# Optimization experiments

Measured on AMD Instinct MI355X. Metric: run time of the kernel, lower is better.

## Reference

```python
import jax, jax.numpy as jnp
import numpy as np

N_NODES = 50000
N_EDGES = 800000
IN_CH = 64
HID = 64
EDGE_DIM = 16


def _glorot(key, shape):
    fan_in, fan_out = shape[0], shape[1]
    lim = (6.0 / (fan_in + fan_out)) ** 0.5
    return jax.random.uniform(key, shape, jnp.float32, -lim, lim)


def setup_inputs() -> dict:
    key = jax.random.key(0)
    ks = jax.random.split(key, 12)
    x = jax.random.normal(ks[0], (N_NODES, IN_CH), jnp.float32)
    edge_index = jax.random.randint(ks[1], (2, N_EDGES), 0, N_NODES, jnp.int64)
    edge_attr = jax.random.normal(ks[2], (N_EDGES, EDGE_DIM), jnp.float32)
    # SAGEConv1: lin_l (aggregated neighbors, with bias) + lin_r (root, no bias)
    W1l = _glorot(ks[3], (IN_CH, HID)); b1l = jnp.zeros((HID,), jnp.float32)
    W1r = _glorot(ks[4], (IN_CH, HID))
    # SAGEConv2
    W2l = _glorot(ks[5], (HID, HID)); b2l = jnp.zeros((HID,), jnp.float32)
    W2r = _glorot(ks[6], (HID, HID))
    # edge MLP: Linear(2*HID+EDGE_DIM -> HID), ReLU, Linear(HID -> 1)
    Wm1 = _glorot(ks[7], (2 * HID + EDGE_DIM, HID))
    bm1 = jnp.zeros((HID,), jnp.float32)
    Wm2 = _glorot(ks[8], (HID, 1))
    bm2 = jnp.zeros((1,), jnp.float32)
    return dict(x=x, edge_index=edge_index, edge_attr=edge_attr,
                W1l=W1l, b1l=b1l, W1r=W1r,
                W2l=W2l, b2l=b2l, W2r=W2r,
                Wm1=Wm1, bm1=bm1, Wm2=Wm2, bm2=bm2)


def _sage_conv(x, src, dst, deg_inv, Wl, bl, Wr):
    # mean aggregation of source-node features at destination nodes
    n = x.shape[0]
    agg = jax.ops.segment_sum(x[src], dst, num_segments=n)  # [N, d]
    agg = agg * deg_inv  # mean over incoming edges
    return agg @ Wl + bl + x @ Wr


def reference(x, edge_index, edge_attr, W1l, b1l, W1r, W2l, b2l, W2r, Wm1, bm1, Wm2, bm2):
    src, dst = edge_index[0], edge_index[1]
    n = x.shape[0]
    # in-degree (over dst), clamped to 1 as in PyG mean aggregation
    deg = jax.ops.segment_sum(jnp.ones((src.shape[0],), x.dtype), dst, num_segments=n)
    deg_inv = (1.0 / jnp.maximum(deg, 1.0))[:, None]  # [N,1]

    h = jax.nn.relu(_sage_conv(x, src, dst, deg_inv, W1l, b1l, W1r))
    h = jax.nn.relu(_sage_conv(h, src, dst, deg_inv, W2l, b2l, W2r))

    # gather endpoint embeddings + concat with edge features -> MLP score
    edge_input = jnp.concatenate([h[src], h[dst], edge_attr], axis=-1)  # [E, 2H+De]
    hidden = jax.nn.relu(edge_input @ Wm1 + bm1)
    return (hidden @ Wm2 + bm2).squeeze(-1)  # [E]
```

## Files before the change

### kernel.cpp

```cpp
#include <hip/hip_runtime.h>
#include <hip/hip_bf16.h>


#define C 64
#define KP 168
#define SK 136
#define TILE_E 64

typedef short short8 __attribute__((ext_vector_type(8)));
typedef float f32x4 __attribute__((ext_vector_type(4)));

__device__ __forceinline__ unsigned short f2bf(float f) {
    unsigned int u = __float_as_uint(f);
    return (unsigned short)((u + 0x7FFFu + ((u >> 16) & 1u)) >> 16);
}
__device__ __forceinline__ unsigned int pack2(float lo, float hi) {
    return (unsigned int)f2bf(lo) | ((unsigned int)f2bf(hi) << 16);
}
__device__ __forceinline__ float bflo(unsigned int u) { return __uint_as_float(u << 16); }
__device__ __forceinline__ float bfhi(unsigned int u) { return __uint_as_float(u & 0xFFFF0000u); }

__global__ void prep(const int* __restrict__ dst, int* __restrict__ degi,
                     const float* __restrict__ ea, unsigned short* __restrict__ eaB,
                     const float* __restrict__ x, unsigned short* __restrict__ xB,
                     int E, int nx8, int doEa) {
    int i = blockIdx.x * blockDim.x + threadIdx.x;
    if (i < E) atomicAdd(&degi[dst[i]], 1);
    if (doEa && i < 2 * E) {
        const float4* p = (const float4*)(ea + (size_t)i * 8);
        float4 a = p[0], b = p[1];
        uint4 o;
        o.x = pack2(a.x, a.y); o.y = pack2(a.z, a.w);
        o.z = pack2(b.x, b.y); o.w = pack2(b.z, b.w);
        *(uint4*)(eaB + (size_t)i * 8) = o;
    }
    if (i < nx8) {
        const float4* p = (const float4*)(x + (size_t)i * 8);
        float4 a = p[0], b = p[1];
        uint4 o;
        o.x = pack2(a.x, a.y); o.y = pack2(a.z, a.w);
        o.z = pack2(b.x, b.y); o.w = pack2(b.z, b.w);
        *(uint4*)(xB + (size_t)i * 8) = o;
    }
}

__global__ __launch_bounds__(256) void scan_partial(const int* __restrict__ degi,
        int* __restrict__ rowptr, int* __restrict__ partials, int N) {
    __shared__ int sWs[4];
    int t = threadIdx.x, b = blockIdx.x;
    int g0 = b * 1024 + t * 4;
    int v0 = (g0 + 0 < N) ? degi[g0 + 0] : 0;
    int v1 = (g0 + 1 < N) ? degi[g0 + 1] : 0;
    int v2 = (g0 + 2 < N) ? degi[g0 + 2] : 0;
    int v3 = (g0 + 3 < N) ? degi[g0 + 3] : 0;
    int tsum = v0 + v1 + v2 + v3;
    int lane = t & 63, w = t >> 6;
    int incl = tsum;
    #pragma unroll
    for (int m = 1; m < 64; m <<= 1) {
        int y = __shfl_up(incl, m, 64);
        if (lane >= m) incl += y;
    }
    if (lane == 63) sWs[w] = incl;
    __syncthreads();
    int wprefix = 0;
    for (int i = 0; i < w; ++i) wprefix += sWs[i];
    int run = wprefix + incl - tsum;
    if (g0 + 0 < N) rowptr[g0 + 0] = run; run += v0;
    if (g0 + 1 < N) rowptr[g0 + 1] = run; run += v1;
    if (g0 + 2 < N) rowptr[g0 + 2] = run; run += v2;
    if (g0 + 3 < N) rowptr[g0 + 3] = run;
    if (t == 255) partials[b] = wprefix + incl;
}

__global__ __launch_bounds__(256) void scan_add_fused(int* __restrict__ rowptr,
        const int* __restrict__ partials, int* __restrict__ cursor,
        const int* __restrict__ degi, float* __restrict__ deg_inv,
        int N, int E, int nb) {
    __shared__ int sOff[64];
    int t = threadIdx.x;
    if (t < 64) {
        int v = (t < nb) ? partials[t] : 0;
        int incl = v;
        #pragma unroll
        for (int m = 1; m < 64; m <<= 1) {
            int y = __shfl_up(incl, m, 64);
            if (t >= m) incl += y;
        }
        sOff[t] = incl - v;
    }
    __syncthreads();
    int i = blockIdx.x * 256 + t;
    if (i < N) {
        int r = rowptr[i] + sOff[i >> 10];
        rowptr[i] = r;
        cursor[i] = r;
        deg_inv[i] = 1.0f / fmaxf((float)degi[i], 1.0f);
    }
    if (i == 0) rowptr[N] = E;
}

__global__ void fill_csr(const int* __restrict__ src, const int* __restrict__ dst,
                         int* __restrict__ cursor, int* __restrict__ eSrc, int E) {
    int e = blockIdx.x * blockDim.x + threadIdx.x;
    if (e < E) {
        int p = atomicAdd(&cursor[dst[e]], 1);
        eSrc[p] = src[e];
    }
}

__global__ __launch_bounds__(256) void fused_layer(
        const unsigned short* __restrict__ fB,
        const int* __restrict__ rowptr, const int* __restrict__ eSrc,
        const float* __restrict__ deg_inv,
        const float* __restrict__ Wl, const float* __restrict__ Wr,
        const float* __restrict__ bl, unsigned short* __restrict__ hOut, int N) {
    __shared__ unsigned short sW[C * SK];
    __shared__ unsigned short sAB[C * SK];
    int t = threadIdx.x;
    int lane = t & 63, w = t >> 6;
    int l15 = lane & 15, quad = lane >> 4;
    int n0 = blockIdx.x * 64;

    for (int i = t; i < 128 * C; i += 256) {
        int k = i >> 6, n = i & 63;
        float v = (k < C) ? Wl[k * C + n] : Wr[(k - C) * C + n];
        sW[n * SK + k] = f2bf(v);
    }
    for (int i = t; i < 64 * 8; i += 256) {
        int r = i >> 3, ch = i & 7;
        int node = n0 + r;
        uint4 v = {0u, 0u, 0u, 0u};
        if (node < N) v = *(const uint4*)(fB + (size_t)node * C + ch * 8);
        *(uint4*)&sAB[r * SK + 64 + ch * 8] = v;
    }

    int s8 = lane >> 3, ci = lane & 7;
    for (int p = 0; p < 16; ++p) {
        int node = n0 + w * 16 + p;
        if (node >= N) break;
        int row = rowptr[node], end = rowptr[node + 1];
        float a[8] = {0.f, 0.f, 0.f, 0.f, 0.f, 0.f, 0.f, 0.f};
        int j = row;
        for (; j + 16 <= end; j += 16) {
            int sA = eSrc[j + s8];
            int sB = eSrc[j + 8 + s8];
            uint4 vA = *(const uint4*)(fB + (size_t)sA * C + ci * 8);
            uint4 vB = *(const uint4*)(fB + (size_t)sB * C + ci * 8);
            a[0] += bflo(vA.x); a[1] += bfhi(vA.x);
            a[2] += bflo(vA.y); a[3] += bfhi(vA.y);
            a[4] += bflo(vA.z); a[5] += bfhi(vA.z);
            a[6] += bflo(vA.w); a[7] += bfhi(vA.w);
            a[0] += bflo(vB.x); a[1] += bfhi(vB.x);
            a[2] += bflo(vB.y); a[3] += bfhi(vB.y);
            a[4] += bflo(vB.z); a[5] += bfhi(vB.z);
            a[6] += bflo(vB.w); a[7] += bfhi(vB.w);
        }
        for (; j < end; j += 8) {
            if (j + s8 < end) {
                int s = eSrc[j + s8];
                uint4 v = *(const uint4*)(fB + (size_t)s * C + ci * 8);
                a[0] += bflo(v.x); a[1] += bfhi(v.x);
                a[2] += bflo(v.y); a[3] += bfhi(v.y);
                a[4] += bflo(v.z); a[5] += bfhi(v.z);
                a[6] += bflo(v.w); a[7] += bfhi(v.w);
            }
        }
        #pragma unroll
        for (int m = 8; m < 64; m <<= 1)
            #pragma unroll
            for (int k = 0; k < 8; ++k)
                a[k] += __shfl_xor(a[k], m, 64);
        if (s8 == 0) {
            float di = deg_inv[node];
            uint4 o;
            o.x = pack2(a[0] * di, a[1] * di);
            o.y = pack2(a[2] * di, a[3] * di);
            o.z = pack2(a[4] * di, a[5] * di);
            o.w = pack2(a[6] * di, a[7] * di);
            *(uint4*)&sAB[(w * 16 + p) * SK + ci * 8] = o;
        }
    }
    __syncthreads();

    short8 bW[4][4];
    #pragma unroll
    for (int t4 = 0; t4 < 4; ++t4)
        #pragma unroll
        for (int kc = 0; kc < 4; ++kc)
            bW[t4][kc] = *(const short8*)&sW[(t4 * 16 + l15) * SK + kc * 32 + quad * 8];
    float blr[4];
    #pragma unroll
    for (int t4 = 0; t4 < 4; ++t4) blr[t4] = bl[t4 * 16 + l15];

    f32x4 acc[4] = {{0.f, 0.f, 0.f, 0.f}, {0.f, 0.f, 0.f, 0.f},
                    {0.f, 0.f, 0.f, 0.f}, {0.f, 0.f, 0.f, 0.f}};
    #pragma unroll
    for (int kc = 0; kc < 4; ++kc) {
        short8 a = *(const short8*)&sAB[(w * 16 + l15) * SK + kc * 32 + quad * 8];
        #pragma unroll
        for (int t4 = 0; t4 < 4; ++t4)
            acc[t4] = __builtin_amdgcn_mfma_f32_16x16x32_bf16(a, bW[t4][kc], acc[t4], 0, 0, 0);
    }
    __syncthreads();

    #pragma unroll
    for (int t4 = 0; t4 < 4; ++t4)
        #pragma unroll
        for (int r = 0; r < 4; ++r) {
            int rl = w * 16 + quad * 4 + r;
            sW[rl * 72 + t4 * 16 + l15] = f2bf(fmaxf(acc[t4][r] + blr[t4], 0.f));
        }
    __syncthreads();
    for (int i = t; i < 64 * 8; i += 256) {
        int r = i >> 3, c8 = i & 7;
        int node = n0 + r;
        if (node < N)
            *(uint4*)(hOut + (size_t)node * C + c8 * 8) = *(const uint4*)&sW[r * 72 + c8 * 8];
    }
}

template <bool EAB>
__device__ __forceinline__ void gather_rows(const unsigned short* __restrict__ hB,
        const unsigned short* __restrict__ eaB, const float* __restrict__ ea,
        int s, int d, int idxc, int quad,
        uint4& u0, uint4& u1, uint4& u2, uint4& u3, uint4& u4) {
    const uint4* ps = (const uint4*)(hB + (size_t)s * C);
    const uint4* pd = (const uint4*)(hB + (size_t)d * C);
    u0 = ps[quad];
    u1 = ps[4 + quad];
    u2 = pd[quad];
    u3 = pd[4 + quad];
    u4.x = 0u; u4.y = 0u; u4.z = 0u; u4.w = 0u;
    if (quad < 2) {
        if (EAB) {
            u4 = *(const uint4*)(eaB + (size_t)idxc * 16 + quad * 8);
        } else {
            const float4* pe = (const float4*)(ea + (size_t)idxc * 16 + quad * 8);
            float4 f0 = pe[0], f1 = pe[1];
            u4.x = pack2(f0.x, f0.y); u4.y = pack2(f0.z, f0.w);
            u4.z = pack2(f1.x, f1.y); u4.w = pack2(f1.z, f1.w);
        }
    }
}

template <bool EAB>
__global__ __launch_bounds__(256) void edge_mlp_pipe(
        const unsigned short* __restrict__ hB, const int* __restrict__ src,
        const int* __restrict__ dst, const float* __restrict__ ea,
        const unsigned short* __restrict__ eaB,
        const float* __restrict__ Wm1, const float* __restrict__ bm1,
        const float* __restrict__ Wm2, const float* __restrict__ bm2,
        float* __restrict__ out, int E, int nTiles) {
    __shared__ unsigned short sW[C * KP];
    int t = threadIdx.x;
    int lane = t & 63, w = t >> 6;
    int l15 = lane & 15, quad = lane >> 4;

    for (int i = t; i < C * 3; i += 256) {
        int r = i / 3, cc = 144 + (i % 3) * 8;
        uint4 z = {0u, 0u, 0u, 0u};
        *(uint4*)&sW[r * KP + cc] = z;
    }
    for (int i = t; i < 144 * C; i += 256) {
        int k = i >> 6, n = i & 63;
        sW[n * KP + k] = f2bf(Wm1[i]);
    }
    __syncthreads();

    short8 bW[4][5];
    #pragma unroll
    for (int t4 = 0; t4 < 4; ++t4)
        #pragma unroll
        for (int kc = 0; kc < 5; ++kc)
            bW[t4][kc] = *(const short8*)&sW[(t4 * 16 + l15) * KP + kc * 32 + quad * 8];
    float bmr[4], w2r[4];
    #pragma unroll
    for (int t4 = 0; t4 < 4; ++t4) {
        int j = t4 * 16 + l15;
        bmr[t4] = bm1[j];
        w2r[t4] = Wm2[j];
    }
    float bb = bm2[0];

    int stride = gridDim.x;
    int lbase = w * 16 + l15;

    int tile = blockIdx.x;
    int idxc = min(tile * TILE_E + lbase, E - 1);
    int s = src[idxc], d = dst[idxc];
    int tileN = tile + stride;
    int idxNc = (tileN < nTiles) ? min(tileN * TILE_E + lbase, E - 1) : idxc;
    int sN = src[idxNc], dN = dst[idxNc];
    uint4 cu0, cu1, cu2, cu3, cu4;
    gather_rows<EAB>(hB, eaB, ea, s, d, idxc, quad, cu0, cu1, cu2, cu3, cu4);

    while (true) {
        bool hasNext = (tileN < nTiles);
        uint4 nu0, nu1, nu2, nu3, nu4;
        gather_rows<EAB>(hB, eaB, ea, sN, dN, idxNc, quad, nu0, nu1, nu2, nu3, nu4);
        int tileNN = tileN + stride;
        int idxNNc = (tileNN < nTiles) ? min(tileNN * TILE_E + lbase, E - 1) : idxNc;
        int sNN = src[idxNNc], dNN = dst[idxNNc];

        short8 a0 = *(short8*)&cu0, a1 = *(short8*)&cu1, a2 = *(short8*)&cu2,
               a3 = *(short8*)&cu3, a4 = *(short8*)&cu4;
        f32x4 acc[4] = {{0.f, 0.f, 0.f, 0.f}, {0.f, 0.f, 0.f, 0.f},
                        {0.f, 0.f, 0.f, 0.f}, {0.f, 0.f, 0.f, 0.f}};
        #pragma unroll
        for (int t4 = 0; t4 < 4; ++t4) {
            acc[t4] = __builtin_amdgcn_mfma_f32_16x16x32_bf16(a0, bW[t4][0], acc[t4], 0, 0, 0);
            acc[t4] = __builtin_amdgcn_mfma_f32_16x16x32_bf16(a1, bW[t4][1], acc[t4], 0, 0, 0);
            acc[t4] = __builtin_amdgcn_mfma_f32_16x16x32_bf16(a2, bW[t4][2], acc[t4], 0, 0, 0);
            acc[t4] = __builtin_amdgcn_mfma_f32_16x16x32_bf16(a3, bW[t4][3], acc[t4], 0, 0, 0);
            acc[t4] = __builtin_amdgcn_mfma_f32_16x16x32_bf16(a4, bW[t4][4], acc[t4], 0, 0, 0);
        }

        float sres[4];
        #pragma unroll
        for (int r = 0; r < 4; ++r) {
            float v = 0.f;
            #pragma unroll
            for (int t4 = 0; t4 < 4; ++t4)
                v += fmaxf(acc[t4][r] + bmr[t4], 0.f) * w2r[t4];
            #pragma unroll
            for (int m = 1; m < 16; m <<= 1)
                v += __shfl_xor(v, m, 16);
            sres[r] = v;
        }
        if (l15 == 0) {
            int e0 = tile * TILE_E;
            #pragma unroll
            for (int r = 0; r < 4; ++r) {
                int e = e0 + w * 16 + quad * 4 + r;
                if (e < E) out[e] = sres[r] + bb;
            }
        }

        if (!hasNext) break;
        tile = tileN; tileN = tileNN;
        idxc = idxNc; idxNc = idxNNc;
        s = sN; sN = sNN; d = dN; dN = dNN;
        cu0 = nu0; cu1 = nu1; cu2 = nu2; cu3 = nu3; cu4 = nu4;
    }
}

extern "C" void kernel_launch(void* const* d_in, const int* in_sizes, int n_in,
                              void* d_out, int out_size, void* d_ws, size_t ws_size,
                              hipStream_t stream) {
    const float* x   = (const float*)d_in[0];
    const int*   ei  = (const int*)d_in[1];
    const float* ea  = (const float*)d_in[2];
    const float* W1l = (const float*)d_in[3];
    const float* b1l = (const float*)d_in[4];
    const float* W1r = (const float*)d_in[5];
    const float* W2l = (const float*)d_in[6];
    const float* b2l = (const float*)d_in[7];
    const float* W2r = (const float*)d_in[8];
    const float* Wm1 = (const float*)d_in[9];
    const float* bm1 = (const float*)d_in[10];
    const float* Wm2 = (const float*)d_in[11];
    const float* bm2 = (const float*)d_in[12];
    float* out = (float*)d_out;

    const int N = in_sizes[0] / C;
    const int E = in_sizes[1] / 2;
    const int* src = ei;
    const int* dst = ei + E;

    char* wsb = (char*)d_ws;
    int npad = (N + 1023) & ~1023;
    float* deg_inv = (float*)wsb;                wsb += (size_t)npad * 4;
    unsigned short* xB   = (unsigned short*)wsb; wsb += (size_t)npad * C * 2;
    unsigned short* h1B  = (unsigned short*)wsb; wsb += (size_t)npad * C * 2;
    unsigned short* h2B  = (unsigned short*)wsb; wsb += (size_t)npad * C * 2;
    int* degi    = (int*)wsb;                    wsb += (size_t)npad * 4;
    int* rowptr  = (int*)wsb;                    wsb += (size_t)(npad + 64) * 4;
    int* cursor  = (int*)wsb;                    wsb += (size_t)npad * 4;
    int* eSrc    = (int*)wsb;                    wsb += (size_t)E * 4;
    int* partials = (int*)wsb;                   wsb += 64 * 4;
    unsigned short* eaB = (unsigned short*)wsb;
    size_t used = (size_t)(wsb - (char*)d_ws);
    int useEaB = (ws_size >= used + (size_t)E * 16 * 2) ? 1 : 0;

    int tpb = 256;
    int nb = (N + 1023) / 1024;
    int nx8 = N * C / 8;

    hipMemsetAsync(degi, 0, (size_t)N * sizeof(int), stream);
    int prepN = (2 * E > nx8) ? 2 * E : nx8;
    prep<<<(prepN + tpb - 1) / tpb, tpb, 0, stream>>>(dst, degi, ea, eaB, x, xB, E, nx8, useEaB);
    scan_partial<<<nb, tpb, 0, stream>>>(degi, rowptr, partials, N);
    scan_add_fused<<<(N + tpb - 1) / tpb, tpb, 0, stream>>>(rowptr, partials, cursor,
            degi, deg_inv, N, E, nb);
    fill_csr<<<(E + tpb - 1) / tpb, tpb, 0, stream>>>(src, dst, cursor, eSrc, E);

    fused_layer<<<(N + 63) / 64, tpb, 0, stream>>>(xB, rowptr, eSrc, deg_inv,
            W1l, W1r, b1l, h1B, N);
    fused_layer<<<(N + 63) / 64, tpb, 0, stream>>>(h1B, rowptr, eSrc, deg_inv,
            W2l, W2r, b2l, h2B, N);

    int nTiles = (E + TILE_E - 1) / TILE_E;
    int grid = nTiles < 2048 ? nTiles : 2048;
    if (useEaB)
        edge_mlp_pipe<true><<<grid, tpb, 0, stream>>>(h2B, src, dst, ea, eaB,
                Wm1, bm1, Wm2, bm2, out, E, nTiles);
    else
        edge_mlp_pipe<false><<<grid, tpb, 0, stream>>>(h2B, src, dst, ea, eaB,
                Wm1, bm1, Wm2, bm2, out, E, nTiles);
}
```

Before: 333.8 us.

## Split fused SAGE layer into CSR aggregation and MFMA dense kernels; windowed CSR fill

The fused per-layer kernel, which had each 64-node block aggregate its neighbours serially per wave before the MFMA, is split in two. One kernel gives each wave a single node for the bf16 gather-mean and writes the result to a new buffer. A separate MFMA kernel then reads the aggregate and the root features. CSR fill now makes several passes over the edges, each handling one window of destination nodes, to localise the atomics and scattered writes. This raises parallelism in the gather stage, but adds an intermediate round-trip through global memory, extra kernel launches, and rereads of the edge list for every window.

```diff
diff --git a/kernel.cpp b/kernel.cpp
--- a/kernel.cpp
+++ b/kernel.cpp
@@ -100,19 +100,77 @@
     if (i == 0) rowptr[N] = E;
 }
 
-__global__ void fill_csr(const int* __restrict__ src, const int* __restrict__ dst,
-                         int* __restrict__ cursor, int* __restrict__ eSrc, int E) {
-    int e = blockIdx.x * blockDim.x + threadIdx.x;
-    if (e < E) {
-        int p = atomicAdd(&cursor[dst[e]], 1);
-        eSrc[p] = src[e];
-    }
-}
-
-__global__ __launch_bounds__(256) void fused_layer(
-        const unsigned short* __restrict__ fB,
+#define WSHIFT 14
+__global__ __launch_bounds__(256) void fill_csr_win(const int* __restrict__ src,
+        const int* __restrict__ dst, int* __restrict__ cursor,
+        int* __restrict__ eSrc, int E, int npass) {
+    int tid0 = blockIdx.x * blockDim.x + threadIdx.x;
+    int stride = gridDim.x * blockDim.x;
+    for (int p = 0; p < npass; ++p) {
+        int lo = p << WSHIFT;
+        int hi = lo + (1 << WSHIFT);
+        for (int e = tid0; e < E; e += stride) {
+            int d = dst[e];
+            if (d >= lo && d < hi) {
+                int pos = atomicAdd(&cursor[d], 1);
+                eSrc[pos] = src[e];
+            }
+        }
+    }
+}
+
+__global__ __launch_bounds__(256) void csr_agg_bf16(const unsigned short* __restrict__ fB,
         const int* __restrict__ rowptr, const int* __restrict__ eSrc,
-        const float* __restrict__ deg_inv,
+        const float* __restrict__ deg_inv, unsigned short* __restrict__ aggB, int N) {
+    int node = blockIdx.x * 4 + (threadIdx.x >> 6);
+    if (node >= N) return;
+    int lane = threadIdx.x & 63;
+    int s8 = lane >> 3, ci = lane & 7;
+    int row = rowptr[node], end = rowptr[node + 1];
+    float a[8] = {0.f, 0.f, 0.f, 0.f, 0.f, 0.f, 0.f, 0.f};
+    int j = row;
+    for (; j + 16 <= end; j += 16) {
+        int sA = eSrc[j + s8];
+        int sB = eSrc[j + 8 + s8];
+        uint4 vA = *(const uint4*)(fB + (size_t)sA * C + ci * 8);
+        uint4 vB = *(const uint4*)(fB + (size_t)sB * C + ci * 8);
+        a[0] += bflo(vA.x); a[1] += bfhi(vA.x);
+        a[2] += bflo(vA.y); a[3] += bfhi(vA.y);
+        a[4] += bflo(vA.z); a[5] += bfhi(vA.z);
+        a[6] += bflo(vA.w); a[7] += bfhi(vA.w);
+        a[0] += bflo(vB.x); a[1] += bfhi(vB.x);
+        a[2] += bflo(vB.y); a[3] += bfhi(vB.y);
+        a[4] += bflo(vB.z); a[5] += bfhi(vB.z);
+        a[6] += bflo(vB.w); a[7] += bfhi(vB.w);
+    }
+    for (; j < end; j += 8) {
+        if (j + s8 < end) {
+            int s = eSrc[j + s8];
+            uint4 v = *(const uint4*)(fB + (size_t)s * C + ci * 8);
+            a[0] += bflo(v.x); a[1] += bfhi(v.x);
+            a[2] += bflo(v.y); a[3] += bfhi(v.y);
+            a[4] += bflo(v.z); a[5] += bfhi(v.z);
+            a[6] += bflo(v.w); a[7] += bfhi(v.w);
+        }
+    }
+    #pragma unroll
+    for (int m = 8; m < 64; m <<= 1)
+        #pragma unroll
+        for (int k = 0; k < 8; ++k)
+            a[k] += __shfl_xor(a[k], m, 64);
+    if (s8 == 0) {
+        float di = deg_inv[node];
+        uint4 o;
+        o.x = pack2(a[0] * di, a[1] * di);
+        o.y = pack2(a[2] * di, a[3] * di);
+        o.z = pack2(a[4] * di, a[5] * di);
+        o.w = pack2(a[6] * di, a[7] * di);
+        *(uint4*)(aggB + (size_t)node * C + ci * 8) = o;
+    }
+}
+
+__global__ __launch_bounds__(256) void dense_mfma(
+        const unsigned short* __restrict__ aB, const unsigned short* __restrict__ xB,
         const float* __restrict__ Wl, const float* __restrict__ Wr,
         const float* __restrict__ bl, unsigned short* __restrict__ hOut, int N) {
     __shared__ unsigned short sW[C * SK];
@@ -127,59 +185,14 @@
         float v = (k < C) ? Wl[k * C + n] : Wr[(k - C) * C + n];
         sW[n * SK + k] = f2bf(v);
     }
-    for (int i = t; i < 64 * 8; i += 256) {
-        int r = i >> 3, ch = i & 7;
+    for (int i = t; i < 64 * 16; i += 256) {
+        int r = i >> 4, ch = i & 15;
         int node = n0 + r;
         uint4 v = {0u, 0u, 0u, 0u};
-        if (node < N) v = *(const uint4*)(fB + (size_t)node * C + ch * 8);
-        *(uint4*)&sAB[r * SK + 64 + ch * 8] = v;
-    }
-
-    int s8 = lane >> 3, ci = lane & 7;
-    for (int p = 0; p < 16; ++p) {
-        int node = n0 + w * 16 + p;
-        if (node >= N) break;
-        int row = rowptr[node], end = rowptr[node + 1];
-        float a[8] = {0.f, 0.f, 0.f, 0.f, 0.f, 0.f, 0.f, 0.f};
-        int j = row;
-        for (; j + 16 <= end; j += 16) {
-            int sA = eSrc[j + s8];
-            int sB = eSrc[j + 8 + s8];
-            uint4 vA = *(const uint4*)(fB + (size_t)sA * C + ci * 8);
-            uint4 vB = *(const uint4*)(fB + (size_t)sB * C + ci * 8);
-            a[0] += bflo(vA.x); a[1] += bfhi(vA.x);
-            a[2] += bflo(vA.y); a[3] += bfhi(vA.y);
-            a[4] += bflo(vA.z); a[5] += bfhi(vA.z);
-            a[6] += bflo(vA.w); a[7] += bfhi(vA.w);
-            a[0] += bflo(vB.x); a[1] += bfhi(vB.x);
-            a[2] += bflo(vB.y); a[3] += bfhi(vB.y);
-            a[4] += bflo(vB.z); a[5] += bfhi(vB.z);
-            a[6] += bflo(vB.w); a[7] += bfhi(vB.w);
-        }
-        for (; j < end; j += 8) {
-            if (j + s8 < end) {
-                int s = eSrc[j + s8];
-                uint4 v = *(const uint4*)(fB + (size_t)s * C + ci * 8);
-                a[0] += bflo(v.x); a[1] += bfhi(v.x);
-                a[2] += bflo(v.y); a[3] += bfhi(v.y);
-                a[4] += bflo(v.z); a[5] += bfhi(v.z);
-                a[6] += bflo(v.w); a[7] += bfhi(v.w);
-            }
-        }
-        #pragma unroll
-        for (int m = 8; m < 64; m <<= 1)
-            #pragma unroll
-            for (int k = 0; k < 8; ++k)
-                a[k] += __shfl_xor(a[k], m, 64);
-        if (s8 == 0) {
-            float di = deg_inv[node];
-            uint4 o;
-            o.x = pack2(a[0] * di, a[1] * di);
-            o.y = pack2(a[2] * di, a[3] * di);
-            o.z = pack2(a[4] * di, a[5] * di);
-            o.w = pack2(a[6] * di, a[7] * di);
-            *(uint4*)&sAB[(w * 16 + p) * SK + ci * 8] = o;
-        }
+        if (node < N)
+            v = (ch < 8) ? *(const uint4*)(aB + (size_t)node * C + ch * 8)
+                         : *(const uint4*)(xB + (size_t)node * C + (ch - 8) * 8);
+        *(uint4*)&sAB[r * SK + ch * 8] = v;
     }
     __syncthreads();
 
@@ -374,6 +387,7 @@
     unsigned short* xB   = (unsigned short*)wsb; wsb += (size_t)npad * C * 2;
     unsigned short* h1B  = (unsigned short*)wsb; wsb += (size_t)npad * C * 2;
     unsigned short* h2B  = (unsigned short*)wsb; wsb += (size_t)npad * C * 2;
+    unsigned short* aggB = (unsigned short*)wsb; wsb += (size_t)npad * C * 2;
     int* degi    = (int*)wsb;                    wsb += (size_t)npad * 4;
     int* rowptr  = (int*)wsb;                    wsb += (size_t)(npad + 64) * 4;
     int* cursor  = (int*)wsb;                    wsb += (size_t)npad * 4;
@@ -393,12 +407,14 @@
     scan_partial<<<nb, tpb, 0, stream>>>(degi, rowptr, partials, N);
     scan_add_fused<<<(N + tpb - 1) / tpb, tpb, 0, stream>>>(rowptr, partials, cursor,
             degi, deg_inv, N, E, nb);
-    fill_csr<<<(E + tpb - 1) / tpb, tpb, 0, stream>>>(src, dst, cursor, eSrc, E);
-
-    fused_layer<<<(N + 63) / 64, tpb, 0, stream>>>(xB, rowptr, eSrc, deg_inv,
-            W1l, W1r, b1l, h1B, N);
-    fused_layer<<<(N + 63) / 64, tpb, 0, stream>>>(h1B, rowptr, eSrc, deg_inv,
-            W2l, W2r, b2l, h2B, N);
+    int npass = (N + (1 << WSHIFT) - 1) >> WSHIFT;
+    fill_csr_win<<<1024, tpb, 0, stream>>>(src, dst, cursor, eSrc, E, npass);
+
+    csr_agg_bf16<<<(N + 3) / 4, tpb, 0, stream>>>(xB, rowptr, eSrc, deg_inv, aggB, N);
+    dense_mfma<<<(N + 63) / 64, tpb, 0, stream>>>(aggB, xB, W1l, W1r, b1l, h1B, N);
+
+    csr_agg_bf16<<<(N + 3) / 4, tpb, 0, stream>>>(h1B, rowptr, eSrc, deg_inv, aggB, N);
+    dense_mfma<<<(N + 63) / 64, tpb, 0, stream>>>(aggB, h1B, W2l, W2r, b2l, h2B, N);
 
     int nTiles = (E + TILE_E - 1) / TILE_E;
     int grid = nTiles < 2048 ? nTiles : 2048;
```

Measured after the change: 308.8 us. -7.5%, faster.
